# Optimization experiments

Hardware: AMD Instinct MI355X
Metric: run time of the kernel (lower is better)

The kernel has to match this reference:

```python
import jax, jax.numpy as jnp
import numpy as np

N_NODES = 50000
N_EDGES = 500000
IN_CH = 128
OUT_CH = 64
HEADS = 4


def setup_inputs() -> dict:
    key = jax.random.key(0)
    ks = jax.random.split(key, 9)
    x = jax.random.normal(ks[0], (N_NODES, IN_CH), dtype=jnp.float32)
    edge_index = jax.random.randint(ks[1], (2, N_EDGES), 0, N_NODES, dtype=jnp.int64)
    edge_weights = jax.random.uniform(ks[2], (N_EDGES, 1), dtype=jnp.float32)
    # xavier-uniform params, stored as [in, out] so y = x @ W
    def xavier(k, shape):
        fan_in, fan_out = shape
        lim = float(np.sqrt(6.0 / (fan_in + fan_out)))
        return jax.random.uniform(k, shape, minval=-lim, maxval=lim, dtype=jnp.float32)
    Wq = xavier(ks[3], (IN_CH, OUT_CH * HEADS))
    Wk = xavier(ks[4], (IN_CH, OUT_CH * HEADS))
    Wv = xavier(ks[5], (IN_CH, OUT_CH * HEADS))
    We = xavier(ks[6], (1, HEADS))
    Wout = xavier(ks[7], (OUT_CH * HEADS, OUT_CH))
    b_out = jnp.zeros((OUT_CH,), dtype=jnp.float32)
    return {"x": x, "edge_index": edge_index, "edge_weights": edge_weights,
            "Wq": Wq, "Wk": Wk, "Wv": Wv, "We": We, "Wout": Wout, "b_out": b_out}


def reference(x, edge_index, edge_weights, Wq, Wk, Wv, We, Wout, b_out):
    num_nodes = x.shape[0]
    src = edge_index[0]
    tgt = edge_index[1]
    x_src = x[src]                                    # [E, in]
    x_tgt = x[tgt]                                    # [E, in]
    q = (x_tgt @ Wq).reshape(-1, HEADS, OUT_CH)       # [E, H, C]
    k = (x_src @ Wk).reshape(-1, HEADS, OUT_CH)
    v = (x_src @ Wv).reshape(-1, HEADS, OUT_CH)
    attn = jnp.sum(q * k, axis=-1) / jnp.sqrt(jnp.float32(OUT_CH))  # [E, H]
    attn = attn + edge_weights @ We                   # [E, H]
    attn = jax.nn.leaky_relu(attn, negative_slope=0.2)
    attn = jax.nn.softmax(attn, axis=0)               # global softmax over edges (as in source)
    weighted_v = attn[..., None] * v                  # [E, H, C]
    out = jax.ops.segment_sum(weighted_v, tgt, num_segments=num_nodes)  # [N, H, C]
    out = out.reshape(num_nodes, HEADS * OUT_CH) @ Wout + b_out         # [N, out]
    if x.shape == out.shape:
        out = out + x
    return out
```

## Files before the change

kernel.cpp:

```cpp
#include <hip/hip_runtime.h>
#include <hip/hip_bf16.h>
#include <hip/hip_fp16.h>

#define N_NODES 50000
#define N_EDGES 500000
#define IN_CH   128
#define D       256
#define UDIM    512
#define OUT_CH  64
#define HEADS   4
#define NC      49

typedef _Float16 half8 __attribute__((ext_vector_type(8)));
typedef float   floatx4 __attribute__((ext_vector_type(4)));

__global__ __launch_bounds__(256) void init_kernel(int* __restrict__ cnt,
                                                   double* __restrict__ S) {
    int i = blockIdx.x * 256 + threadIdx.x;
    if (i < N_NODES) cnt[i] = 0;
    if (i < HEADS) S[i] = 0.0;
}

__global__ __launch_bounds__(256) void x16_kernel(const float* __restrict__ x,
                                                  __half* __restrict__ x16) {
    int i = (blockIdx.x * 256 + threadIdx.x) * 4;
    if (i < N_NODES * IN_CH) {
        float4 v = *(const float4*)(x + i);
        union { __half2 h[2]; uint2 u; } pk;
        pk.h[0] = __floats2half2_rn(v.x, v.y);
        pk.h[1] = __floats2half2_rn(v.z, v.w);
        *(uint2*)(x16 + i) = pk.u;
    }
}

__global__ __launch_bounds__(128) void mbuild_kernel(const float* __restrict__ Wq,
                                                     const float* __restrict__ Wk,
                                                     __half* __restrict__ M16t) {
    const int r = blockIdx.x;
    const int h = r >> 7, j = r & 127;
    const int i = threadIdx.x;
    __shared__ float kj[64];
    if (i < 64) kj[i] = Wk[(size_t)j * D + h * 64 + i];
    __syncthreads();
    const float4* qr = (const float4*)(Wq + (size_t)i * D + h * 64);
    float s = 0.f;
    #pragma unroll
    for (int c4 = 0; c4 < 16; ++c4) {
        float4 q = qr[c4];
        s += q.x * kj[c4 * 4] + q.y * kj[c4 * 4 + 1]
           + q.z * kj[c4 * 4 + 2] + q.w * kj[c4 * 4 + 3];
    }
    M16t[(size_t)r * IN_CH + i] = __float2half(s);
}

__global__ __launch_bounds__(64) void zbuild_kernel(const float* __restrict__ Wv,
                                                    const float* __restrict__ Wout,
                                                    __half* __restrict__ Zc16t) {
    const int r = blockIdx.x;
    const int h = r >> 7, i = r & 127;
    const int c = threadIdx.x;
    __shared__ float vi[64];
    vi[c] = Wv[(size_t)i * D + h * 64 + c];
    __syncthreads();
    float s = 0.f;
    #pragma unroll 8
    for (int j = 0; j < 64; ++j)
        s += vi[j] * Wout[(size_t)(h * 64 + j) * OUT_CH + c];
    Zc16t[(size_t)c * UDIM + r] = __float2half(s);
}

__global__ __launch_bounds__(256) void gemm_u_mfma_kernel(const __half* __restrict__ x16,
                                                          const __half* __restrict__ M16t,
                                                          __half* __restrict__ u16) {
    __shared__ __half Ax[128][136];
    __shared__ __half Bm[128][136];
    const int m0 = blockIdx.x * 128;
    const int colbase = blockIdx.y * 128;
    const int tid = threadIdx.x;

    {
        const int r = tid >> 1, part = tid & 1;
        uint4 va[8];
        if (m0 + r < N_NODES) {
            const uint4* src = (const uint4*)(x16 + (size_t)(m0 + r) * IN_CH + part * 64);
            #pragma unroll
            for (int q = 0; q < 8; ++q) va[q] = src[q];
        } else {
            #pragma unroll
            for (int q = 0; q < 8; ++q) va[q] = make_uint4(0u, 0u, 0u, 0u);
        }
        uint4* da = (uint4*)&Ax[r][part * 64];
        #pragma unroll
        for (int q = 0; q < 8; ++q) da[q] = va[q];
        const uint4* sb = (const uint4*)(M16t + (size_t)(colbase + r) * IN_CH + part * 64);
        uint4* db = (uint4*)&Bm[r][part * 64];
        #pragma unroll
        for (int q = 0; q < 8; ++q) db[q] = sb[q];
    }
    __syncthreads();

    const int w = tid >> 6, lane = tid & 63;
    const int mrow = lane & 15, quad = lane >> 4;

    half8 a[2][4];
    #pragma unroll
    for (int mt = 0; mt < 2; ++mt)
        #pragma unroll
        for (int ks = 0; ks < 4; ++ks)
            a[mt][ks] = *(const half8*)&Ax[w * 32 + mt * 16 + mrow][ks * 32 + quad * 8];

    floatx4 acc[2][8];
    #pragma unroll
    for (int mt = 0; mt < 2; ++mt)
        #pragma unroll
        for (int nt = 0; nt < 8; ++nt)
            acc[mt][nt] = (floatx4){0.f, 0.f, 0.f, 0.f};

    #pragma unroll
    for (int nt = 0; nt < 8; ++nt) {
        #pragma unroll
        for (int ks = 0; ks < 4; ++ks) {
            half8 b = *(const half8*)&Bm[nt * 16 + mrow][ks * 32 + quad * 8];
            acc[0][nt] = __builtin_amdgcn_mfma_f32_16x16x32_f16(a[0][ks], b, acc[0][nt], 0, 0, 0);
            acc[1][nt] = __builtin_amdgcn_mfma_f32_16x16x32_f16(a[1][ks], b, acc[1][nt], 0, 0, 0);
        }
    }
    __syncthreads();
    #pragma unroll
    for (int mt = 0; mt < 2; ++mt)
        #pragma unroll
        for (int nt = 0; nt < 8; ++nt)
            #pragma unroll
            for (int r = 0; r < 4; ++r)
                Ax[w * 32 + mt * 16 + quad * 4 + r][nt * 16 + mrow] = __float2half(acc[mt][nt][r]);
    __syncthreads();
    {
        const int r = tid >> 1, part = tid & 1;
        if (m0 + r < N_NODES) {
            const uint4* s4 = (const uint4*)&Ax[r][part * 64];
            uint4* d4 = (uint4*)(u16 + (size_t)(m0 + r) * UDIM + colbase + part * 64);
            #pragma unroll
            for (int q = 0; q < 8; ++q) d4[q] = s4[q];
        }
    }
}

__global__ __launch_bounds__(256) void hist_kernel(const int* __restrict__ ei,
                                                   int* __restrict__ cnt) {
    int e = blockIdx.x * 256 + threadIdx.x;
    if (e < N_EDGES) atomicAdd(&cnt[ei[N_EDGES + e]], 1);
}

__global__ __launch_bounds__(256) void scan_reduce_kernel(const int* __restrict__ cnt,
                                                          int* __restrict__ csum) {
    const int b = blockIdx.x, tid = threadIdx.x;
    const int lane = tid & 63, wid = tid >> 6;
    int s = 0;
    int idx0 = b * 1024 + tid * 4;
    #pragma unroll
    for (int i = 0; i < 4; ++i) {
        int idx = idx0 + i;
        if (idx < N_NODES) s += cnt[idx];
    }
    #pragma unroll
    for (int m = 1; m < 64; m <<= 1) s += __shfl_xor(s, m, 64);
    __shared__ int w[4];
    if (lane == 0) w[wid] = s;
    __syncthreads();
    if (tid == 0) csum[b] = w[0] + w[1] + w[2] + w[3];
}

__global__ __launch_bounds__(64) void scan_top_kernel(int* __restrict__ csum) {
    int lane = threadIdx.x;
    int v = (lane < NC) ? csum[lane] : 0;
    int x = v;
    #pragma unroll
    for (int d = 1; d < 64; d <<= 1) {
        int y = __shfl_up(x, d, 64);
        if (lane >= d) x += y;
    }
    if (lane < NC) csum[lane] = x - v;
}

__global__ __launch_bounds__(256) void scan_chunks_kernel(int* __restrict__ cnt,
                                                          const int* __restrict__ csum,
                                                          int* __restrict__ rp) {
    const int b = blockIdx.x, tid = threadIdx.x;
    const int lane = tid & 63, wid = tid >> 6;
    __shared__ int wsum[4];
    int v[4];
    const int idx0 = b * 1024 + tid * 4;
    #pragma unroll
    for (int i = 0; i < 4; ++i) {
        int idx = idx0 + i;
        v[i] = (idx < N_NODES) ? cnt[idx] : 0;
    }
    int tsum = v[0] + v[1] + v[2] + v[3];
    int x = tsum;
    #pragma unroll
    for (int d = 1; d < 64; d <<= 1) {
        int y = __shfl_up(x, d, 64);
        if (lane >= d) x += y;
    }
    if (lane == 63) wsum[wid] = x;
    __syncthreads();
    int woff = 0;
    for (int w = 0; w < wid; ++w) woff += wsum[w];
    int excl = csum[b] + woff + x - tsum;
    #pragma unroll
    for (int i = 0; i < 4; ++i) {
        int idx = idx0 + i;
        if (idx < N_NODES) { rp[idx] = excl; cnt[idx] = excl; }
        excl += v[i];
    }
}

__global__ __launch_bounds__(256) void scatter_kernel(const int* __restrict__ ei,
                                                      const float* __restrict__ ew,
                                                      int* __restrict__ cnt,
                                                      int2* __restrict__ payload) {
    int e = blockIdx.x * 256 + threadIdx.x;
    if (e >= N_EDGES) return;
    int s = ei[e], t = ei[N_EDGES + e];
    int pos = atomicAdd(&cnt[t], 1);
    payload[pos] = make_int2(s, __float_as_int(ew[e]));
}

__global__ __launch_bounds__(256) void edge_fused_kernel(const __half* __restrict__ u16,
                                                         const __half* __restrict__ x16,
                                                         const int* __restrict__ rp,
                                                         const int* __restrict__ cnt,
                                                         const int2* __restrict__ payload,
                                                         const float* __restrict__ We,
                                                         __half* __restrict__ y16,
                                                         double* __restrict__ S) {
    const int tid = threadIdx.x;
    const int j = tid & 15;
    const int node = blockIdx.x * 16 + (tid >> 4);
    const float4 we = *(const float4*)We;
    const float wev[4] = {we.x, we.y, we.z, we.w};

    const __half* ur = u16 + (size_t)node * UDIM;
    float4 ua[4], ub[4], ya[4], yb[4];
    #pragma unroll
    for (int h = 0; h < 4; ++h) {
        uint4 raw = *(const uint4*)(ur + h * 128 + j * 8);
        const __half2* hp = (const __half2*)&raw;
        float2 f0 = __half22float2(hp[0]), f1 = __half22float2(hp[1]);
        float2 f2 = __half22float2(hp[2]), f3 = __half22float2(hp[3]);
        ua[h] = make_float4(f0.x, f0.y, f1.x, f1.y);
        ub[h] = make_float4(f2.x, f2.y, f3.x, f3.y);
        ya[h] = make_float4(0.f, 0.f, 0.f, 0.f);
        yb[h] = make_float4(0.f, 0.f, 0.f, 0.f);
    }

    float sacc[4] = {0.f, 0.f, 0.f, 0.f};
    const int start = rp[node];
    const int end = cnt[node];
    int2 pl = (start < end) ? payload[start] : make_int2(0, 0);
    for (int e = start; e < end; ++e) {
        int2 plnext = (e + 1 < end) ? payload[e + 1] : pl;
        const int s = pl.x;
        const float w = __int_as_float(pl.y);
        uint4 raw = *(const uint4*)(x16 + (size_t)s * IN_CH + j * 8);
        const __half2* hp = (const __half2*)&raw;
        float2 f0 = __half22float2(hp[0]), f1 = __half22float2(hp[1]);
        float2 f2 = __half22float2(hp[2]), f3 = __half22float2(hp[3]);
        float4 xa = make_float4(f0.x, f0.y, f1.x, f1.y);
        float4 xb = make_float4(f2.x, f2.y, f3.x, f3.y);
        float d[4];
        #pragma unroll
        for (int h = 0; h < 4; ++h) {
            d[h] = ua[h].x * xa.x + ua[h].y * xa.y + ua[h].z * xa.z + ua[h].w * xa.w
                 + ub[h].x * xb.x + ub[h].y * xb.y + ub[h].z * xb.z + ub[h].w * xb.w;
        }
        #pragma unroll
        for (int m = 1; m < 16; m <<= 1) {
            #pragma unroll
            for (int h = 0; h < 4; ++h) d[h] += __shfl_xor(d[h], m, 16);
        }
        float p[4];
        #pragma unroll
        for (int h = 0; h < 4; ++h) {
            float l = d[h] * 0.125f + w * wev[h];
            l = (l > 0.f) ? l : 0.2f * l;
            p[h] = __expf(l);
        }
        #pragma unroll
        for (int h = 0; h < 4; ++h) {
            ya[h].x += p[h] * xa.x; ya[h].y += p[h] * xa.y;
            ya[h].z += p[h] * xa.z; ya[h].w += p[h] * xa.w;
            yb[h].x += p[h] * xb.x; yb[h].y += p[h] * xb.y;
            yb[h].z += p[h] * xb.z; yb[h].w += p[h] * xb.w;
        }
        if (j == 0) {
            sacc[0] += p[0]; sacc[1] += p[1]; sacc[2] += p[2]; sacc[3] += p[3];
        }
        pl = plnext;
    }
    __half* yr = y16 + (size_t)node * UDIM;
    #pragma unroll
    for (int h = 0; h < 4; ++h) {
        union { __half2 hh[4]; uint4 u; } pk;
        pk.hh[0] = __floats2half2_rn(ya[h].x, ya[h].y);
        pk.hh[1] = __floats2half2_rn(ya[h].z, ya[h].w);
        pk.hh[2] = __floats2half2_rn(yb[h].x, yb[h].y);
        pk.hh[3] = __floats2half2_rn(yb[h].z, yb[h].w);
        *(uint4*)(yr + h * 128 + j * 8) = pk.u;
    }
    __shared__ float sblk[4];
    if (tid < 4) sblk[tid] = 0.f;
    __syncthreads();
    if (j == 0) {
        atomicAdd(&sblk[0], sacc[0]);
        atomicAdd(&sblk[1], sacc[1]);
        atomicAdd(&sblk[2], sacc[2]);
        atomicAdd(&sblk[3], sacc[3]);
    }
    __syncthreads();
    if (tid < 4) atomicAdd(&S[tid], (double)sblk[tid]);
}

__global__ __launch_bounds__(256) void gemm_out_mfma_kernel(const __half* __restrict__ y16,
                                                            const __half* __restrict__ Zc16t,
                                                            const double* __restrict__ S,
                                                            const float* __restrict__ b_out,
                                                            float* __restrict__ out) {
    __shared__ __half Ay[128][136];
    __shared__ __half Bz[64][136];
    __shared__ float invs_s[4];
    const int m0 = blockIdx.x * 128;
    const int tid = threadIdx.x;
    if (tid < 4) invs_s[tid] = (float)(1.0 / S[tid]);

    const int w = tid >> 6, lane = tid & 63;
    const int mrow = lane & 15, quad = lane >> 4;

    floatx4 result[2][4];
    #pragma unroll
    for (int mt = 0; mt < 2; ++mt)
        #pragma unroll
        for (int nt = 0; nt < 4; ++nt)
            result[mt][nt] = (floatx4){0.f, 0.f, 0.f, 0.f};

    for (int h = 0; h < HEADS; ++h) {
        {
            const int r = tid >> 1, part = tid & 1;
            uint4 va[8];
            if (m0 + r < N_NODES) {
                const uint4* src = (const uint4*)(y16 + (size_t)(m0 + r) * UDIM + h * 128 + part * 64);
                #pragma unroll
                for (int q = 0; q < 8; ++q) va[q] = src[q];
            } else {
                #pragma unroll
                for (int q = 0; q < 8; ++q) va[q] = make_uint4(0u, 0u, 0u, 0u);
            }
            uint4* da = (uint4*)&Ay[r][part * 64];
            #pragma unroll
            for (int q = 0; q < 8; ++q) da[q] = va[q];
        }
        {
            const int r = tid >> 2, part = tid & 3;
            const uint4* sb = (const uint4*)(Zc16t + (size_t)r * UDIM + h * 128 + part * 32);
            uint4* db = (uint4*)&Bz[r][part * 32];
            #pragma unroll
            for (int q = 0; q < 4; ++q) db[q] = sb[q];
        }
        __syncthreads();

        half8 a[2][4];
        #pragma unroll
        for (int mt = 0; mt < 2; ++mt)
            #pragma unroll
            for (int ks = 0; ks < 4; ++ks)
                a[mt][ks] = *(const half8*)&Ay[w * 32 + mt * 16 + mrow][ks * 32 + quad * 8];

        floatx4 acc[2][4];
        #pragma unroll
        for (int mt = 0; mt < 2; ++mt)
            #pragma unroll
            for (int nt = 0; nt < 4; ++nt)
                acc[mt][nt] = (floatx4){0.f, 0.f, 0.f, 0.f};

        #pragma unroll
        for (int nt = 0; nt < 4; ++nt) {
            #pragma unroll
            for (int ks = 0; ks < 4; ++ks) {
                half8 b = *(const half8*)&Bz[nt * 16 + mrow][ks * 32 + quad * 8];
                acc[0][nt] = __builtin_amdgcn_mfma_f32_16x16x32_f16(a[0][ks], b, acc[0][nt], 0, 0, 0);
                acc[1][nt] = __builtin_amdgcn_mfma_f32_16x16x32_f16(a[1][ks], b, acc[1][nt], 0, 0, 0);
            }
        }
        const float inv = invs_s[h];
        #pragma unroll
        for (int mt = 0; mt < 2; ++mt)
            #pragma unroll
            for (int nt = 0; nt < 4; ++nt) {
                result[mt][nt][0] += inv * acc[mt][nt][0];
                result[mt][nt][1] += inv * acc[mt][nt][1];
                result[mt][nt][2] += inv * acc[mt][nt][2];
                result[mt][nt][3] += inv * acc[mt][nt][3];
            }
        __syncthreads();
    }
    float bcol[4];
    #pragma unroll
    for (int nt = 0; nt < 4; ++nt) bcol[nt] = b_out[nt * 16 + mrow];
    #pragma unroll
    for (int mt = 0; mt < 2; ++mt) {
        #pragma unroll
        for (int r = 0; r < 4; ++r) {
            int row = m0 + w * 32 + mt * 16 + quad * 4 + r;
            if (row < N_NODES) {
                float* dst = out + (size_t)row * OUT_CH;
                #pragma unroll
                for (int nt = 0; nt < 4; ++nt)
                    dst[nt * 16 + mrow] = result[mt][nt][r] + bcol[nt];
            }
        }
    }
}

extern "C" void kernel_launch(void* const* d_in, const int* in_sizes, int n_in,
                              void* d_out, int out_size, void* d_ws, size_t ws_size,
                              hipStream_t stream) {
    const float* x     = (const float*)d_in[0];
    const int*   ei    = (const int*)d_in[1];
    const float* ew    = (const float*)d_in[2];
    const float* Wq    = (const float*)d_in[3];
    const float* Wk    = (const float*)d_in[4];
    const float* Wv    = (const float*)d_in[5];
    const float* We    = (const float*)d_in[6];
    const float* Wout  = (const float*)d_in[7];
    const float* b_out = (const float*)d_in[8];
    float* out = (float*)d_out;

    __half* u16   = (__half*)d_ws;
    __half* y16   = u16 + (size_t)N_NODES * UDIM;
    __half* x16   = y16 + (size_t)N_NODES * UDIM;
    double* S     = (double*)(x16 + (size_t)N_NODES * IN_CH);
    __half* M16t  = (__half*)(S + HEADS);
    __half* Zc16t = M16t + UDIM * IN_CH;
    int*    rp    = (int*)(Zc16t + OUT_CH * UDIM);
    int*    cnt   = rp + N_NODES;
    int*    csum  = cnt + N_NODES;
    int2*   payload = (int2*)(csum + 64);

    init_kernel<<<(N_NODES + 255) / 256, 256, 0, stream>>>(cnt, S);
    x16_kernel<<<(N_NODES * IN_CH / 4 + 255) / 256, 256, 0, stream>>>(x, x16);
    mbuild_kernel<<<512, 128, 0, stream>>>(Wq, Wk, M16t);
    zbuild_kernel<<<512, 64, 0, stream>>>(Wv, Wout, Zc16t);
    gemm_u_mfma_kernel<<<dim3((N_NODES + 127) / 128, 4), 256, 0, stream>>>(x16, M16t, u16);
    hist_kernel<<<(N_EDGES + 255) / 256, 256, 0, stream>>>(ei, cnt);
    scan_reduce_kernel<<<NC, 256, 0, stream>>>(cnt, csum);
    scan_top_kernel<<<1, 64, 0, stream>>>(csum);
    scan_chunks_kernel<<<NC, 256, 0, stream>>>(cnt, csum, rp);
    scatter_kernel<<<(N_EDGES + 255) / 256, 256, 0, stream>>>(ei, ew, cnt, payload);
    edge_fused_kernel<<<N_NODES / 16, 256, 0, stream>>>(u16, x16, rp, cnt, payload, We, y16, S);
    gemm_out_mfma_kernel<<<(N_NODES + 127) / 128, 256, 0, stream>>>(y16, Zc16t, S, b_out, out);
}
```

Before: 282.2 us.

## Remap edge kernel lanes per head with packed fp16 dot and accumulate

The edge kernel now gives each lane one head and a 32-element slice, so the dot product needs only a 4-lane shuffle reduction instead of 16 lanes times four heads. It computes with fdot2 packed-half instructions, accumulates the weighted sum in fp16 half2 registers, and prefetches the next source row. Separately, the init and cast kernels are merged, as are the two weight-build kernels, to cut launches. Accumulating in fp16 risks precision loss and overflow on high-degree nodes, and each lane now loads 64 bytes per edge rather than 16.

```diff
diff --git a/kernel.cpp b/kernel.cpp
--- a/kernel.cpp
+++ b/kernel.cpp
@@ -12,61 +12,61 @@
 #define NC      49
 
 typedef _Float16 half8 __attribute__((ext_vector_type(8)));
+typedef _Float16 half2_t __attribute__((ext_vector_type(2)));
 typedef float   floatx4 __attribute__((ext_vector_type(4)));
 
-__global__ __launch_bounds__(256) void init_kernel(int* __restrict__ cnt,
+__global__ __launch_bounds__(256) void prep_kernel(const float* __restrict__ x,
+                                                   __half* __restrict__ x16,
+                                                   int* __restrict__ cnt,
                                                    double* __restrict__ S) {
     int i = blockIdx.x * 256 + threadIdx.x;
     if (i < N_NODES) cnt[i] = 0;
     if (i < HEADS) S[i] = 0.0;
-}
-
-__global__ __launch_bounds__(256) void x16_kernel(const float* __restrict__ x,
-                                                  __half* __restrict__ x16) {
-    int i = (blockIdx.x * 256 + threadIdx.x) * 4;
-    if (i < N_NODES * IN_CH) {
-        float4 v = *(const float4*)(x + i);
+    int k = i * 4;
+    if (k < N_NODES * IN_CH) {
+        float4 v = *(const float4*)(x + k);
         union { __half2 h[2]; uint2 u; } pk;
         pk.h[0] = __floats2half2_rn(v.x, v.y);
         pk.h[1] = __floats2half2_rn(v.z, v.w);
-        *(uint2*)(x16 + i) = pk.u;
-    }
-}
-
-__global__ __launch_bounds__(128) void mbuild_kernel(const float* __restrict__ Wq,
+        *(uint2*)(x16 + k) = pk.u;
+    }
+}
+
+__global__ __launch_bounds__(128) void wbuild_kernel(const float* __restrict__ Wq,
                                                      const float* __restrict__ Wk,
-                                                     __half* __restrict__ M16t) {
-    const int r = blockIdx.x;
-    const int h = r >> 7, j = r & 127;
-    const int i = threadIdx.x;
-    __shared__ float kj[64];
-    if (i < 64) kj[i] = Wk[(size_t)j * D + h * 64 + i];
-    __syncthreads();
-    const float4* qr = (const float4*)(Wq + (size_t)i * D + h * 64);
-    float s = 0.f;
-    #pragma unroll
-    for (int c4 = 0; c4 < 16; ++c4) {
-        float4 q = qr[c4];
-        s += q.x * kj[c4 * 4] + q.y * kj[c4 * 4 + 1]
-           + q.z * kj[c4 * 4 + 2] + q.w * kj[c4 * 4 + 3];
-    }
-    M16t[(size_t)r * IN_CH + i] = __float2half(s);
-}
-
-__global__ __launch_bounds__(64) void zbuild_kernel(const float* __restrict__ Wv,
-                                                    const float* __restrict__ Wout,
-                                                    __half* __restrict__ Zc16t) {
-    const int r = blockIdx.x;
-    const int h = r >> 7, i = r & 127;
-    const int c = threadIdx.x;
-    __shared__ float vi[64];
-    vi[c] = Wv[(size_t)i * D + h * 64 + c];
-    __syncthreads();
-    float s = 0.f;
-    #pragma unroll 8
-    for (int j = 0; j < 64; ++j)
-        s += vi[j] * Wout[(size_t)(h * 64 + j) * OUT_CH + c];
-    Zc16t[(size_t)c * UDIM + r] = __float2half(s);
+                                                     const float* __restrict__ Wv,
+                                                     const float* __restrict__ Wout,
+                                                     __half* __restrict__ M16t,
+                                                     __half* __restrict__ Zc16t) {
+    __shared__ float buf[64];
+    const int tid = threadIdx.x;
+    if (blockIdx.x < 512) {
+        const int r = blockIdx.x;
+        const int h = r >> 7, j = r & 127;
+        if (tid < 64) buf[tid] = Wk[(size_t)j * D + h * 64 + tid];
+        __syncthreads();
+        const float4* qr = (const float4*)(Wq + (size_t)tid * D + h * 64);
+        float s = 0.f;
+        #pragma unroll
+        for (int c4 = 0; c4 < 16; ++c4) {
+            float4 q = qr[c4];
+            s += q.x * buf[c4 * 4] + q.y * buf[c4 * 4 + 1]
+               + q.z * buf[c4 * 4 + 2] + q.w * buf[c4 * 4 + 3];
+        }
+        M16t[(size_t)r * IN_CH + tid] = __float2half(s);
+    } else {
+        const int r = blockIdx.x - 512;
+        const int h = r >> 7, i = r & 127;
+        if (tid < 64) buf[tid] = Wv[(size_t)i * D + h * 64 + tid];
+        __syncthreads();
+        if (tid < 64) {
+            float s = 0.f;
+            #pragma unroll 8
+            for (int j = 0; j < 64; ++j)
+                s += buf[j] * Wout[(size_t)(h * 64 + j) * OUT_CH + tid];
+            Zc16t[(size_t)tid * UDIM + r] = __float2half(s);
+        }
+    }
 }
 
 __global__ __launch_bounds__(256) void gemm_u_mfma_kernel(const __half* __restrict__ x16,
@@ -235,88 +235,68 @@
                                                          __half* __restrict__ y16,
                                                          double* __restrict__ S) {
     const int tid = threadIdx.x;
-    const int j = tid & 15;
+    const int l16 = tid & 15;
+    const int h = l16 >> 2;
+    const int q = l16 & 3;
     const int node = blockIdx.x * 16 + (tid >> 4);
-    const float4 we = *(const float4*)We;
-    const float wev[4] = {we.x, we.y, we.z, we.w};
-
-    const __half* ur = u16 + (size_t)node * UDIM;
-    float4 ua[4], ub[4], ya[4], yb[4];
-    #pragma unroll
-    for (int h = 0; h < 4; ++h) {
-        uint4 raw = *(const uint4*)(ur + h * 128 + j * 8);
-        const __half2* hp = (const __half2*)&raw;
-        float2 f0 = __half22float2(hp[0]), f1 = __half22float2(hp[1]);
-        float2 f2 = __half22float2(hp[2]), f3 = __half22float2(hp[3]);
-        ua[h] = make_float4(f0.x, f0.y, f1.x, f1.y);
-        ub[h] = make_float4(f2.x, f2.y, f3.x, f3.y);
-        ya[h] = make_float4(0.f, 0.f, 0.f, 0.f);
-        yb[h] = make_float4(0.f, 0.f, 0.f, 0.f);
-    }
-
-    float sacc[4] = {0.f, 0.f, 0.f, 0.f};
+    const float wev = We[h];
+
+    uint4 ur[4];
+    {
+        const uint4* ub = (const uint4*)(u16 + (size_t)node * UDIM + h * 128 + q * 32);
+        ur[0] = ub[0]; ur[1] = ub[1]; ur[2] = ub[2]; ur[3] = ub[3];
+    }
+    const half2_t* uh = (const half2_t*)ur;
+
+    half2_t yacc[16];
+    #pragma unroll
+    for (int t = 0; t < 16; ++t) yacc[t] = (half2_t){(_Float16)0.f, (_Float16)0.f};
+
+    float sacc = 0.f;
     const int start = rp[node];
     const int end = cnt[node];
-    int2 pl = (start < end) ? payload[start] : make_int2(0, 0);
+    int2 pl = make_int2(0, 0);
+    uint4 xr[4];
+    if (start < end) {
+        pl = payload[start];
+        const uint4* xb = (const uint4*)(x16 + (size_t)pl.x * IN_CH + q * 32);
+        xr[0] = xb[0]; xr[1] = xb[1]; xr[2] = xb[2]; xr[3] = xb[3];
+    }
     for (int e = start; e < end; ++e) {
-        int2 plnext = (e + 1 < end) ? payload[e + 1] : pl;
-        const int s = pl.x;
-        const float w = __int_as_float(pl.y);
-        uint4 raw = *(const uint4*)(x16 + (size_t)s * IN_CH + j * 8);
-        const __half2* hp = (const __half2*)&raw;
-        float2 f0 = __half22float2(hp[0]), f1 = __half22float2(hp[1]);
-        float2 f2 = __half22float2(hp[2]), f3 = __half22float2(hp[3]);
-        float4 xa = make_float4(f0.x, f0.y, f1.x, f1.y);
-        float4 xb = make_float4(f2.x, f2.y, f3.x, f3.y);
-        float d[4];
-        #pragma unroll
-        for (int h = 0; h < 4; ++h) {
-            d[h] = ua[h].x * xa.x + ua[h].y * xa.y + ua[h].z * xa.z + ua[h].w * xa.w
-                 + ub[h].x * xb.x + ub[h].y * xb.y + ub[h].z * xb.z + ub[h].w * xb.w;
-        }
-        #pragma unroll
-        for (int m = 1; m < 16; m <<= 1) {
-            #pragma unroll
-            for (int h = 0; h < 4; ++h) d[h] += __shfl_xor(d[h], m, 16);
-        }
-        float p[4];
-        #pragma unroll
-        for (int h = 0; h < 4; ++h) {
-            float l = d[h] * 0.125f + w * wev[h];
-            l = (l > 0.f) ? l : 0.2f * l;
-            p[h] = __expf(l);
-        }
-        #pragma unroll
-        for (int h = 0; h < 4; ++h) {
-            ya[h].x += p[h] * xa.x; ya[h].y += p[h] * xa.y;
-            ya[h].z += p[h] * xa.z; ya[h].w += p[h] * xa.w;
-            yb[h].x += p[h] * xb.x; yb[h].y += p[h] * xb.y;
-            yb[h].z += p[h] * xb.z; yb[h].w += p[h] * xb.w;
-        }
-        if (j == 0) {
-            sacc[0] += p[0]; sacc[1] += p[1]; sacc[2] += p[2]; sacc[3] += p[3];
-        }
-        pl = plnext;
-    }
-    __half* yr = y16 + (size_t)node * UDIM;
-    #pragma unroll
-    for (int h = 0; h < 4; ++h) {
-        union { __half2 hh[4]; uint4 u; } pk;
-        pk.hh[0] = __floats2half2_rn(ya[h].x, ya[h].y);
-        pk.hh[1] = __floats2half2_rn(ya[h].z, ya[h].w);
-        pk.hh[2] = __floats2half2_rn(yb[h].x, yb[h].y);
-        pk.hh[3] = __floats2half2_rn(yb[h].z, yb[h].w);
-        *(uint4*)(yr + h * 128 + j * 8) = pk.u;
+        int2 pln = pl;
+        uint4 xrn[4] = {xr[0], xr[1], xr[2], xr[3]};
+        if (e + 1 < end) {
+            pln = payload[e + 1];
+            const uint4* xb = (const uint4*)(x16 + (size_t)pln.x * IN_CH + q * 32);
+            xrn[0] = xb[0]; xrn[1] = xb[1]; xrn[2] = xb[2]; xrn[3] = xb[3];
+        }
+        const half2_t* xh = (const half2_t*)xr;
+        float dot = 0.f;
+        #pragma unroll
+        for (int t = 0; t < 16; ++t)
+            dot = __builtin_amdgcn_fdot2(uh[t], xh[t], dot, false);
+        dot += __shfl_xor(dot, 1, 16);
+        dot += __shfl_xor(dot, 2, 16);
+        float l = dot * 0.125f + __int_as_float(pl.y) * wev;
+        l = fmaxf(l, 0.2f * l);
+        float p = __expf(l);
+        if (q == 0) sacc += p;
+        half2_t p2 = (half2_t){(_Float16)p, (_Float16)p};
+        #pragma unroll
+        for (int t = 0; t < 16; ++t)
+            yacc[t] = p2 * xh[t] + yacc[t];
+        pl = pln;
+        xr[0] = xrn[0]; xr[1] = xrn[1]; xr[2] = xrn[2]; xr[3] = xrn[3];
+    }
+    {
+        uint4* yo = (uint4*)(y16 + (size_t)node * UDIM + h * 128 + q * 32);
+        const uint4* ys = (const uint4*)yacc;
+        yo[0] = ys[0]; yo[1] = ys[1]; yo[2] = ys[2]; yo[3] = ys[3];
     }
     __shared__ float sblk[4];
     if (tid < 4) sblk[tid] = 0.f;
     __syncthreads();
-    if (j == 0) {
-        atomicAdd(&sblk[0], sacc[0]);
-        atomicAdd(&sblk[1], sacc[1]);
-        atomicAdd(&sblk[2], sacc[2]);
-        atomicAdd(&sblk[3], sacc[3]);
-    }
+    if (q == 0) atomicAdd(&sblk[h], sacc);
     __syncthreads();
     if (tid < 4) atomicAdd(&S[tid], (double)sblk[tid]);
 }
@@ -350,21 +330,21 @@
             if (m0 + r < N_NODES) {
                 const uint4* src = (const uint4*)(y16 + (size_t)(m0 + r) * UDIM + h * 128 + part * 64);
                 #pragma unroll
-                for (int q = 0; q < 8; ++q) va[q] = src[q];
+                for (int qq = 0; qq < 8; ++qq) va[qq] = src[qq];
             } else {
                 #pragma unroll
-                for (int q = 0; q < 8; ++q) va[q] = make_uint4(0u, 0u, 0u, 0u);
+                for (int qq = 0; qq < 8; ++qq) va[qq] = make_uint4(0u, 0u, 0u, 0u);
             }
             uint4* da = (uint4*)&Ay[r][part * 64];
             #pragma unroll
-            for (int q = 0; q < 8; ++q) da[q] = va[q];
+            for (int qq = 0; qq < 8; ++qq) da[qq] = va[qq];
         }
         {
             const int r = tid >> 2, part = tid & 3;
             const uint4* sb = (const uint4*)(Zc16t + (size_t)r * UDIM + h * 128 + part * 32);
             uint4* db = (uint4*)&Bz[r][part * 32];
             #pragma unroll
-            for (int q = 0; q < 4; ++q) db[q] = sb[q];
+            for (int qq = 0; qq < 4; ++qq) db[qq] = sb[qq];
         }
         __syncthreads();
 
@@ -446,10 +426,8 @@
     int*    csum  = cnt + N_NODES;
     int2*   payload = (int2*)(csum + 64);
 
-    init_kernel<<<(N_NODES + 255) / 256, 256, 0, stream>>>(cnt, S);
-    x16_kernel<<<(N_NODES * IN_CH / 4 + 255) / 256, 256, 0, stream>>>(x, x16);
-    mbuild_kernel<<<512, 128, 0, stream>>>(Wq, Wk, M16t);
-    zbuild_kernel<<<512, 64, 0, stream>>>(Wv, Wout, Zc16t);
+    prep_kernel<<<(N_NODES * IN_CH / 4 + 255) / 256, 256, 0, stream>>>(x, x16, cnt, S);
+    wbuild_kernel<<<1024, 128, 0, stream>>>(Wq, Wk, Wv, Wout, M16t, Zc16t);
     gemm_u_mfma_kernel<<<dim3((N_NODES + 127) / 128, 4), 256, 0, stream>>>(x16, M16t, u16);
     hist_kernel<<<(N_EDGES + 255) / 256, 256, 0, stream>>>(ei, cnt);
     scan_reduce_kernel<<<NC, 256, 0, stream>>>(cnt, csum);
```

Measured after the change: 272.5 us. 1.04x faster.
